# Performance work log

Hardware: AMD Instinct MI355X
Metric: run time of the kernel (lower is better)

Reference implementation:

```python
import jax, jax.numpy as jnp
import numpy as np

B, TE, T = 128, 256, 200
H, PRE, MEL, R = 256, 128, 80, 5
OUT = MEL * R  # 400


def _gru(x, h, wih, whh, bih, bhh):
    # PyTorch GRUCell math. wih: [3H, in], whh: [3H, H]
    gi = x @ wih.T + bih
    gh = h @ whh.T + bhh
    ir, iz, inn = jnp.split(gi, 3, axis=-1)
    hr, hz, hn = jnp.split(gh, 3, axis=-1)
    r = jax.nn.sigmoid(ir + hr)
    z = jax.nn.sigmoid(iz + hz)
    n = jnp.tanh(inn + r * hn)
    return (1.0 - z) * n + z * h


def setup_inputs() -> dict:
    key = jax.random.key(0)
    ks = jax.random.split(key, 32)
    s = 0.05
    d = {
        "encoder_outputs": jax.random.normal(ks[0], (B, TE, H), jnp.float32),
        "targets": jax.random.normal(ks[1], (B, T, OUT), jnp.float32),
        # prenet (note: prenet input is mel_dim*r = 400 frames fed through Linear(400->256)
        # is not in the original; original hardcodes Linear(256,256) on a 400-dim frame --
        # a bug. We size the first prenet layer to the actual frame dim 400.)
        "prenet_w1": jax.random.normal(ks[2], (H, OUT), jnp.float32) * s,
        "prenet_b1": jnp.zeros((H,), jnp.float32),
        "prenet_w2": jax.random.normal(ks[3], (PRE, H), jnp.float32) * s,
        "prenet_b2": jnp.zeros((PRE,), jnp.float32),
        # attention RNN: GRUCell(256+128, 256)
        "attn_wih": jax.random.normal(ks[4], (3 * H, H + PRE), jnp.float32) * s,
        "attn_whh": jax.random.normal(ks[5], (3 * H, H), jnp.float32) * s,
        "attn_bih": jnp.zeros((3 * H,), jnp.float32),
        "attn_bhh": jnp.zeros((3 * H,), jnp.float32),
        # Bahdanau attention: query layer, memory layer (bias-free), score vector v
        "wq": jax.random.normal(ks[6], (H, H), jnp.float32) * s,
        "wm": jax.random.normal(ks[7], (H, H), jnp.float32) * s,
        "v_attn": jax.random.normal(ks[8], (H,), jnp.float32) * s,
        # proj_to_decoder: Linear(512, 256)
        "wp": jax.random.normal(ks[9], (H, 2 * H), jnp.float32) * s,
        "bp": jnp.zeros((H,), jnp.float32),
        # decoder GRUCell x2 (256,256)
        "g1_wih": jax.random.normal(ks[10], (3 * H, H), jnp.float32) * s,
        "g1_whh": jax.random.normal(ks[11], (3 * H, H), jnp.float32) * s,
        "g1_bih": jnp.zeros((3 * H,), jnp.float32),
        "g1_bhh": jnp.zeros((3 * H,), jnp.float32),
        "g2_wih": jax.random.normal(ks[12], (3 * H, H), jnp.float32) * s,
        "g2_whh": jax.random.normal(ks[13], (3 * H, H), jnp.float32) * s,
        "g2_bih": jnp.zeros((3 * H,), jnp.float32),
        "g2_bhh": jnp.zeros((3 * H,), jnp.float32),
        # proj_to_mel: Linear(256, mel_dim*r)
        "wo": jax.random.normal(ks[14], (OUT, H), jnp.float32) * s,
        "bo": jnp.zeros((OUT,), jnp.float32),
    }
    return d


def reference(encoder_outputs, targets, prenet_w1, prenet_b1, prenet_w2, prenet_b2,
              attn_wih, attn_whh, attn_bih, attn_bhh, wq, wm, v_attn, wp, bp,
              g1_wih, g1_whh, g1_bih, g1_bhh, g2_wih, g2_whh, g2_bih, g2_bhh,
              wo, bo):
    b = encoder_outputs.shape[0]
    # precompute processed memory once (original memory_layer)
    pm = encoder_outputs @ wm.T  # [B, Te, H]

    # teacher-forced previous frames: go-frame (zeros) then targets[:, :-1]
    prev = jnp.concatenate([jnp.zeros((b, 1, OUT), encoder_outputs.dtype),
                            targets[:, :-1]], axis=1)  # [B, T, OUT]
    prev = jnp.swapaxes(prev, 0, 1)  # [T, B, OUT]

    def step(carry, frame):
        attn_h, h1, h2, attn_val = carry
        # prenet (dropout in eval mode -> identity)
        p = jax.nn.relu(frame @ prenet_w1.T + prenet_b1)
        p = jax.nn.relu(p @ prenet_w2.T + prenet_b2)  # [B, 128]
        # attention RNN
        x = jnp.concatenate([p, attn_val], axis=-1)  # [B, 384]
        attn_h = _gru(x, attn_h, attn_wih, attn_whh, attn_bih, attn_bhh)
        # Bahdanau additive attention
        q = attn_h @ wq.T  # [B, H]
        e = jnp.einsum('bth,h->bt', jnp.tanh(pm + q[:, None, :]), v_attn)  # [B, Te]
        align = jax.nn.softmax(e, axis=-1)
        attn_val = jnp.einsum('bt,bth->bh', align, encoder_outputs)
        # decoder RNNs with residual connections
        dec_in = jnp.concatenate([attn_h, attn_val], axis=-1) @ wp.T + bp
        h1 = _gru(dec_in, h1, g1_wih, g1_whh, g1_bih, g1_bhh)
        dec_in = h1 + dec_in
        h2 = _gru(dec_in, h2, g2_wih, g2_whh, g2_bih, g2_bhh)
        dec_in = h2 + dec_in
        out = dec_in @ wo.T + bo  # [B, OUT]
        return (attn_h, h1, h2, attn_val), (out, align)

    z = jnp.zeros((b, H), encoder_outputs.dtype)
    init = (z, z, z, z)
    _, (outs, aligns) = jax.lax.scan(step, init, prev)
    outputs = jnp.swapaxes(outs, 0, 1)      # [B, T, mel_dim*r]
    alignments = jnp.swapaxes(aligns, 0, 1)  # [B, T, Te]
    return outputs, alignments
```

## Files before the change

kernel.cpp:

```cpp
#include <hip/hip_runtime.h>

#define B_    128
#define T_    200
#define TE_   256
#define H_    256
#define PRE_  128
#define OUT_  400
#define BT_   (B_*T_)

__device__ __forceinline__ float sigm_(float x){ return 1.f/(1.f+__expf(-x)); }
__device__ __forceinline__ float tanh_(float x){
  x = fminf(15.f, fmaxf(-15.f, x));
  float e = __expf(2.f*x);
  return 1.f - 2.f/(e+1.f);
}
__device__ __forceinline__ float b2f_lo(unsigned u){ return __uint_as_float(u << 16); }
__device__ __forceinline__ float b2f_hi(unsigned u){ return __uint_as_float(u & 0xffff0000u); }
__device__ __forceinline__ unsigned short f2b(float f){
  unsigned u = __float_as_uint(f);
  unsigned r = (u + 0x7fff + ((u >> 16) & 1)) >> 16;
  return (unsigned short)r;
}

#define Q4(xv, wv, A0,A1,A2,A3) \
  A0=fmaf(xv,b2f_lo(wv.x),A0); A1=fmaf(xv,b2f_hi(wv.x),A1); \
  A2=fmaf(xv,b2f_lo(wv.y),A2); A3=fmaf(xv,b2f_hi(wv.y),A3);

struct TD { const float* src; void* dst; int N; int Ksrc; int col0; int Keff; int bf16; int blk0; };
struct TDs { TD d[14]; };

__global__ __launch_bounds__(256) void transpose_cast(TDs P)
{
  int bid = blockIdx.x, m = 0;
#pragma unroll
  for (int i = 1; i < 14; ++i) if (bid >= P.d[i].blk0) m = i;
  TD t = P.d[m];
  long gid = (long)(bid - t.blk0)*256 + threadIdx.x;
  long nk = (long)t.N * t.Keff;
  if (gid >= nk) return;
  int k = (int)(gid / t.N);
  int j = (int)(gid % t.N);
  float v = t.src[(size_t)j*t.Ksrc + t.col0 + k];
  if (t.bf16) ((unsigned short*)t.dst)[(size_t)k*t.N + j] = f2b(v);
  else        ((float*)t.dst)[(size_t)k*t.N + j] = v;
}

template<int AMODE, bool RELU, int OUTMODE>
__global__ __launch_bounds__(256) void gemm_k(const float* __restrict__ A, int lda,
                                              const float* __restrict__ WT, int N, int K,
                                              const float* __restrict__ bias,
                                              float* __restrict__ C)
{
  const int tid  = threadIdx.x;
  const int row0 = blockIdx.x * 64;
  const int n0   = blockIdx.y * 64;
  __shared__ float As[16][68];
  __shared__ float Bs[16][64];
  const int tx = tid & 15, ty = tid >> 4;
  float acc[4][4];
#pragma unroll
  for (int i = 0; i < 4; ++i)
#pragma unroll
    for (int j = 0; j < 4; ++j) acc[i][j] = 0.f;

  for (int k0 = 0; k0 < K; k0 += 16){
#pragma unroll
    for (int l = 0; l < 4; ++l){
      int idx = tid + l*256;
      int m2 = idx >> 4, kk = idx & 15;
      float v;
      if (AMODE == 1){
        int r = row0 + m2;
        int t = r % T_;
        v = (t == 0) ? 0.f : A[(size_t)(r-1)*OUT_ + k0 + kk];
      } else {
        v = A[(size_t)(row0+m2)*lda + k0 + kk];
      }
      As[kk][m2] = v;
    }
#pragma unroll
    for (int l = 0; l < 4; ++l){
      int idx = tid + l*256;
      int kk = idx >> 6, j = idx & 63;
      int jg = n0 + j;
      Bs[kk][j] = (jg < N) ? WT[(size_t)(k0+kk)*N + jg] : 0.f;
    }
    __syncthreads();
#pragma unroll
    for (int kk = 0; kk < 16; ++kk){
      float4 a4 = *(const float4*)&As[kk][ty*4];
      float4 b4 = *(const float4*)&Bs[kk][tx*4];
      acc[0][0] = fmaf(a4.x, b4.x, acc[0][0]); acc[0][1] = fmaf(a4.x, b4.y, acc[0][1]);
      acc[0][2] = fmaf(a4.x, b4.z, acc[0][2]); acc[0][3] = fmaf(a4.x, b4.w, acc[0][3]);
      acc[1][0] = fmaf(a4.y, b4.x, acc[1][0]); acc[1][1] = fmaf(a4.y, b4.y, acc[1][1]);
      acc[1][2] = fmaf(a4.y, b4.z, acc[1][2]); acc[1][3] = fmaf(a4.y, b4.w, acc[1][3]);
      acc[2][0] = fmaf(a4.z, b4.x, acc[2][0]); acc[2][1] = fmaf(a4.z, b4.y, acc[2][1]);
      acc[2][2] = fmaf(a4.z, b4.z, acc[2][2]); acc[2][3] = fmaf(a4.z, b4.w, acc[2][3]);
      acc[3][0] = fmaf(a4.w, b4.x, acc[3][0]); acc[3][1] = fmaf(a4.w, b4.y, acc[3][1]);
      acc[3][2] = fmaf(a4.w, b4.z, acc[3][2]); acc[3][3] = fmaf(a4.w, b4.w, acc[3][3]);
    }
    __syncthreads();
  }
#pragma unroll
  for (int i = 0; i < 4; ++i){
    int r = row0 + ty*4 + i;
#pragma unroll
    for (int jj = 0; jj < 4; ++jj){
      int c = n0 + tx*4 + jj;
      if (c < N){
        float v = acc[i][jj] + (bias ? bias[c] : 0.f);
        if (RELU) v = fmaxf(v, 0.f);
        if (OUTMODE == 0){
          C[(size_t)r*N + c] = v;
        } else if (OUTMODE == 1){
          int b = r / TE_, te = r % TE_;
          C[((size_t)b*H_ + c)*TE_ + te] = v;
        } else {
          int b = r / TE_, te = r % TE_;
          ((unsigned short*)C)[((size_t)b*H_ + c)*TE_ + te] = f2b(v);
        }
      }
    }
  }
}

__device__ __forceinline__ void mv768_pair(const uint2* __restrict__ wA, const uint2* __restrict__ wB,
                                           const float* __restrict__ xA, const float* __restrict__ xB,
                                           float* __restrict__ outA, float* __restrict__ outB,
                                           int kg, int jt)
{
  const float4* xa4 = (const float4*)xA;
  const float4* xb4 = (const float4*)xB;
  const uint2* pA = wA + (size_t)(kg*64)*192 + jt;
  const uint2* pB = wB + (size_t)(kg*64)*192 + jt;
  float a0=0,a1=0,a2=0,a3=0, c0=0,c1=0,c2=0,c3=0;
#pragma unroll 4
  for (int k4 = 0; k4 < 16; ++k4){
    float4 x1 = xa4[kg*16+k4];
    float4 x2 = xb4[kg*16+k4];
    uint2 wa0=pA[0],wa1=pA[192],wa2=pA[384],wa3=pA[576]; pA += 768;
    uint2 wb0=pB[0],wb1=pB[192],wb2=pB[384],wb3=pB[576]; pB += 768;
    Q4(x1.x, wa0, a0,a1,a2,a3) Q4(x1.y, wa1, a0,a1,a2,a3)
    Q4(x1.z, wa2, a0,a1,a2,a3) Q4(x1.w, wa3, a0,a1,a2,a3)
    Q4(x2.x, wb0, c0,c1,c2,c3) Q4(x2.y, wb1, c0,c1,c2,c3)
    Q4(x2.z, wb2, c0,c1,c2,c3) Q4(x2.w, wb3, c0,c1,c2,c3)
  }
  *(float4*)(outA + jt*4) = make_float4(a0,a1,a2,a3);
  *(float4*)(outB + jt*4) = make_float4(c0,c1,c2,c3);
}

__device__ __forceinline__ void mv768_single(const uint2* __restrict__ w,
                                             const float* __restrict__ x,
                                             float* __restrict__ out, int kg, int jt)
{
  const float4* x4 = (const float4*)x;
  const uint2* p = w + (size_t)(kg*64)*192 + jt;
  float a0=0,a1=0,a2=0,a3=0;
#pragma unroll 4
  for (int k4 = 0; k4 < 16; ++k4){
    float4 x1 = x4[kg*16+k4];
    uint2 w0=p[0],w1=p[192],w2=p[384],w3=p[576]; p += 768;
    Q4(x1.x, w0, a0,a1,a2,a3) Q4(x1.y, w1, a0,a1,a2,a3)
    Q4(x1.z, w2, a0,a1,a2,a3) Q4(x1.w, w3, a0,a1,a2,a3)
  }
  *(float4*)(out + jt*4) = make_float4(a0,a1,a2,a3);
}

__device__ __forceinline__ void mv256_pair(const uint2* __restrict__ wA, const uint2* __restrict__ wB,
                                           const float* __restrict__ x,
                                           float* __restrict__ outA, float* __restrict__ outB,
                                           int kg, int jt)
{
  const float4* x4 = (const float4*)x;
  const uint2* pA = wA + (size_t)(kg*16)*64 + jt;
  const uint2* pB = wB + (size_t)(kg*16)*64 + jt;
  float a0=0,a1=0,a2=0,a3=0, c0=0,c1=0,c2=0,c3=0;
#pragma unroll
  for (int k4 = 0; k4 < 4; ++k4){
    float4 x1 = x4[kg*4+k4];
    uint2 wa0=pA[0],wa1=pA[64],wa2=pA[128],wa3=pA[192]; pA += 256;
    uint2 wb0=pB[0],wb1=pB[64],wb2=pB[128],wb3=pB[192]; pB += 256;
    Q4(x1.x, wa0, a0,a1,a2,a3) Q4(x1.y, wa1, a0,a1,a2,a3)
    Q4(x1.z, wa2, a0,a1,a2,a3) Q4(x1.w, wa3, a0,a1,a2,a3)
    Q4(x1.x, wb0, c0,c1,c2,c3) Q4(x1.y, wb1, c0,c1,c2,c3)
    Q4(x1.z, wb2, c0,c1,c2,c3) Q4(x1.w, wb3, c0,c1,c2,c3)
  }
  *(float4*)(outA + jt*4) = make_float4(a0,a1,a2,a3);
  *(float4*)(outB + jt*4) = make_float4(c0,c1,c2,c3);
}

__device__ __forceinline__ void mv256_single(const uint2* __restrict__ w,
                                             const float* __restrict__ x,
                                             float* __restrict__ out, int kg, int jt)
{
  const float4* x4 = (const float4*)x;
  const uint2* p = w + (size_t)(kg*16)*64 + jt;
  float a0=0,a1=0,a2=0,a3=0;
#pragma unroll
  for (int k4 = 0; k4 < 4; ++k4){
    float4 x1 = x4[kg*4+k4];
    uint2 w0=p[0],w1=p[64],w2=p[128],w3=p[192]; p += 256;
    Q4(x1.x, w0, a0,a1,a2,a3) Q4(x1.y, w1, a0,a1,a2,a3)
    Q4(x1.z, w2, a0,a1,a2,a3) Q4(x1.w, w3, a0,a1,a2,a3)
  }
  *(float4*)(out + jt*4) = make_float4(a0,a1,a2,a3);
}

__device__ __forceinline__ float gru_gate(float gi0,float gi1,float gi2,
                                          float gh0,float gh1,float gh2, float hprev){
  float r = sigm_(gi0+gh0);
  float z = sigm_(gi1+gh1);
  float n = tanh_(gi2 + r*gh2);
  return (1.f-z)*n + z*hprev;
}

struct DP {
  const float *preGI;
  const unsigned short *pm16, *enc16;
  const unsigned short *awihA, *awhh, *wq, *wp, *g1wih, *g1whh, *g2wih, *g2whh;
  const float *abhh, *g1bih, *g1bhh, *g2bih, *g2bhh, *bp, *v_attn;
  float *decbuf, *aln;
};

__global__ __launch_bounds__(1024) void decoder_kernel(DP P)
{
  const int tid = threadIdx.x;
  const int b = blockIdx.x;

  __shared__ __align__(16) float s_part[12288];
  __shared__ __align__(16) float s_g1h[768], s_g2h[768];
  __shared__ __align__(16) float s_ah[H_], s_h1[H_], s_h2[H_], s_av[H_], s_dec[H_];
  __shared__ __align__(16) float s_q[H_], s_dq[H_], s_al[TE_], s_v[H_];
  __shared__ __align__(16) float s_preg[768];
  __shared__ float s_red[4];

  float r_bh0=0,r_bh1=0,r_bh2=0, r_1bi0=0,r_1bi1=0,r_1bi2=0;
  float r_2bi0=0,r_2bi1=0,r_2bi2=0, r_bp=0, r_g1bh=0, r_g2bh=0;
  if (tid < H_){
    r_bh0=P.abhh[tid];  r_bh1=P.abhh[H_+tid];  r_bh2=P.abhh[2*H_+tid];
    r_1bi0=P.g1bih[tid]; r_1bi1=P.g1bih[H_+tid]; r_1bi2=P.g1bih[2*H_+tid];
    r_2bi0=P.g2bih[tid]; r_2bi1=P.g2bih[H_+tid]; r_2bi2=P.g2bih[2*H_+tid];
    r_bp=P.bp[tid];
    s_v[tid]=P.v_attn[tid];
    s_ah[tid]=0.f; s_h1[tid]=0.f; s_h2[tid]=0.f; s_av[tid]=0.f;
  } else {
    int j = tid - 256;
    r_g1bh = P.g1bhh[j];
    r_g2bh = P.g2bhh[j];
  }
  __syncthreads();

  const float* preg = P.preGI + (size_t)b*T_*768;
  const uint2* pm2  = (const uint2*)(P.pm16  + (size_t)b*H_*TE_);
  const uint2* en2  = (const uint2*)(P.enc16 + (size_t)b*TE_*H_);
  float* aln_b = P.aln + (size_t)b*T_*TE_;
  float* dec_b = P.decbuf + (size_t)b*T_*H_;

  const uint2* awihA2 = (const uint2*)P.awihA;
  const uint2* awhh2  = (const uint2*)P.awhh;
  const uint2* wq2    = (const uint2*)P.wq;
  const uint2* wpA2   = (const uint2*)P.wp;
  const uint2* wpB2   = ((const uint2*)P.wp) + 16384;
  const uint2* g1wih2 = (const uint2*)P.g1wih;
  const uint2* g1whh2 = (const uint2*)P.g1whh;
  const uint2* g2wih2 = (const uint2*)P.g2wih;
  const uint2* g2whh2 = (const uint2*)P.g2whh;

  const int kg8 = tid >> 6, jt8 = tid & 63;

  for (int t = 0; t < T_; ++t){
    if (tid < 768){
      const int kg = tid / 192, jt = tid - (tid/192)*192;
      mv768_pair(awihA2, awhh2, s_av, s_ah,
                 s_part + (0*4+kg)*768, s_part + (1*4+kg)*768, kg, jt);
      mv768_pair(g1whh2, g2whh2, s_h1, s_h2,
                 s_part + (2*4+kg)*768, s_part + (3*4+kg)*768, kg, jt);
    } else {
      int i = tid - 768;
      s_preg[i]       = preg[(size_t)t*768 + i];
      s_preg[i + 256] = preg[(size_t)t*768 + i + 256];
      s_preg[i + 512] = preg[(size_t)t*768 + i + 512];
    }
    __syncthreads();
    if (tid < H_){
      float gi0 = s_part[tid]     + s_part[768+tid]     + s_part[1536+tid]     + s_part[2304+tid]     + s_preg[tid];
      float gi1 = s_part[256+tid] + s_part[1024+tid]    + s_part[1792+tid]     + s_part[2560+tid]     + s_preg[256+tid];
      float gi2 = s_part[512+tid] + s_part[1280+tid]    + s_part[2048+tid]     + s_part[2816+tid]     + s_preg[512+tid];
      float gh0 = s_part[3072+tid]     + s_part[3840+tid]     + s_part[4608+tid]     + s_part[5376+tid]     + r_bh0;
      float gh1 = s_part[3072+256+tid] + s_part[3840+256+tid] + s_part[4608+256+tid] + s_part[5376+256+tid] + r_bh1;
      float gh2 = s_part[3072+512+tid] + s_part[3840+512+tid] + s_part[4608+512+tid] + s_part[5376+512+tid] + r_bh2;
      s_ah[tid] = gru_gate(gi0,gi1,gi2, gh0,gh1,gh2, s_ah[tid]);
    } else {
      int j = tid - 256;
      s_g1h[j] = s_part[6144+j] + s_part[6912+j] + s_part[7680+j] + s_part[8448+j] + r_g1bh;
      s_g2h[j] = s_part[9216+j] + s_part[9984+j] + s_part[10752+j] + s_part[11520+j] + r_g2bh;
    }
    __syncthreads();

    mv256_pair(wq2, wpA2, s_ah, s_part + kg8*256, s_part + 4096 + kg8*256, kg8, jt8);
    __syncthreads();
    if (tid < 256){
      float q = 0.f;
#pragma unroll
      for (int g = 0; g < 16; ++g) q += s_part[g*256 + tid];
      s_q[tid] = q;
    } else if (tid < 512){
      int j = tid - 256;
      float d = 0.f;
#pragma unroll
      for (int g = 0; g < 16; ++g) d += s_part[4096 + g*256 + j];
      s_dq[j] = d;
    }
    __syncthreads();

    {
      float a0=0,a1=0,a2=0,a3=0;
#pragma unroll 4
      for (int hh = 0; hh < 16; ++hh){
        int h = kg8*16 + hh;
        uint2 pv = pm2[(size_t)h*64 + jt8];
        float qh = s_q[h], vh = s_v[h];
        a0 = fmaf(vh, tanh_(b2f_lo(pv.x)+qh), a0);
        a1 = fmaf(vh, tanh_(b2f_hi(pv.x)+qh), a1);
        a2 = fmaf(vh, tanh_(b2f_lo(pv.y)+qh), a2);
        a3 = fmaf(vh, tanh_(b2f_hi(pv.y)+qh), a3);
      }
      *(float4*)(s_part + kg8*256 + jt8*4) = make_float4(a0,a1,a2,a3);
    }
    __syncthreads();
    float ex = 0.f;
    if (tid < TE_){
      float e = 0.f;
#pragma unroll
      for (int g = 0; g < 16; ++g) e += s_part[g*256 + tid];
      ex = __expf(e);
      float s = ex;
      for (int o = 32; o; o >>= 1) s += __shfl_down(s, o, 64);
      if ((tid & 63) == 0) s_red[tid >> 6] = s;
    }
    __syncthreads();
    if (tid < TE_){
      float s = (s_red[0]+s_red[1])+(s_red[2]+s_red[3]);
      float al = ex / s;
      s_al[tid] = al;
      aln_b[(size_t)t*TE_ + tid] = al;
    }
    __syncthreads();

    {
      float a0=0,a1=0,a2=0,a3=0;
#pragma unroll 4
      for (int tt = 0; tt < 16; ++tt){
        int te = kg8*16 + tt;
        float alv = s_al[te];
        uint2 ev = en2[(size_t)te*64 + jt8];
        a0 = fmaf(alv, b2f_lo(ev.x), a0);
        a1 = fmaf(alv, b2f_hi(ev.x), a1);
        a2 = fmaf(alv, b2f_lo(ev.y), a2);
        a3 = fmaf(alv, b2f_hi(ev.y), a3);
      }
      *(float4*)(s_part + kg8*256 + jt8*4) = make_float4(a0,a1,a2,a3);
    }
    __syncthreads();
    if (tid < H_){
      float av = 0.f;
#pragma unroll
      for (int g = 0; g < 16; ++g) av += s_part[g*256 + tid];
      s_av[tid] = av;
    }
    __syncthreads();

    mv256_single(wpB2, s_av, s_part + kg8*256, kg8, jt8);
    __syncthreads();
    if (tid < H_){
      float d = s_dq[tid] + r_bp;
#pragma unroll
      for (int g = 0; g < 16; ++g) d += s_part[g*256 + tid];
      s_dec[tid] = d;
    }
    __syncthreads();

    if (tid < 768){
      const int kg = tid / 192, jt = tid - (tid/192)*192;
      mv768_single(g1wih2, s_dec, s_part + kg*768, kg, jt);
    }
    __syncthreads();
    if (tid < H_){
      float gi0 = s_part[tid]     + s_part[768+tid]  + s_part[1536+tid] + s_part[2304+tid] + r_1bi0;
      float gi1 = s_part[256+tid] + s_part[1024+tid] + s_part[1792+tid] + s_part[2560+tid] + r_1bi1;
      float gi2 = s_part[512+tid] + s_part[1280+tid] + s_part[2048+tid] + s_part[2816+tid] + r_1bi2;
      float h1n = gru_gate(gi0,gi1,gi2, s_g1h[tid], s_g1h[256+tid], s_g1h[512+tid], s_h1[tid]);
      s_h1[tid] = h1n;
      s_dec[tid] += h1n;
    }
    __syncthreads();

    if (tid < 768){
      const int kg = tid / 192, jt = tid - (tid/192)*192;
      mv768_single(g2wih2, s_dec, s_part + kg*768, kg, jt);
    }
    __syncthreads();
    if (tid < H_){
      float gi0 = s_part[tid]     + s_part[768+tid]  + s_part[1536+tid] + s_part[2304+tid] + r_2bi0;
      float gi1 = s_part[256+tid] + s_part[1024+tid] + s_part[1792+tid] + s_part[2560+tid] + r_2bi1;
      float gi2 = s_part[512+tid] + s_part[1280+tid] + s_part[2048+tid] + s_part[2816+tid] + r_2bi2;
      float h2n = gru_gate(gi0,gi1,gi2, s_g2h[tid], s_g2h[256+tid], s_g2h[512+tid], s_h2[tid]);
      s_h2[tid] = h2n;
      float d = s_dec[tid] + h2n;
      s_dec[tid] = d;
      dec_b[(size_t)t*H_ + tid] = d;
    }
    __syncthreads();
  }
}

extern "C" void kernel_launch(void* const* d_in, const int* in_sizes, int n_in,
                              void* d_out, int out_size, void* d_ws, size_t ws_size,
                              hipStream_t stream)
{
  const float* enc   = (const float*)d_in[0];
  const float* tgt   = (const float*)d_in[1];
  const float* pw1   = (const float*)d_in[2];
  const float* pb1   = (const float*)d_in[3];
  const float* pw2   = (const float*)d_in[4];
  const float* pb2   = (const float*)d_in[5];
  const float* awih  = (const float*)d_in[6];
  const float* awhh  = (const float*)d_in[7];
  const float* abih  = (const float*)d_in[8];
  const float* abhh  = (const float*)d_in[9];
  const float* wq    = (const float*)d_in[10];
  const float* wm    = (const float*)d_in[11];
  const float* vat   = (const float*)d_in[12];
  const float* wp    = (const float*)d_in[13];
  const float* bp    = (const float*)d_in[14];
  const float* g1wih = (const float*)d_in[15];
  const float* g1whh = (const float*)d_in[16];
  const float* g1bih = (const float*)d_in[17];
  const float* g1bhh = (const float*)d_in[18];
  const float* g2wih = (const float*)d_in[19];
  const float* g2whh = (const float*)d_in[20];
  const float* g2bih = (const float*)d_in[21];
  const float* g2bhh = (const float*)d_in[22];
  const float* wo    = (const float*)d_in[23];
  const float* bo    = (const float*)d_in[24];

  float* ws = (float*)d_ws;
  size_t off = 0;
  auto alloc = [&](size_t n){ float* p = ws + off; off += (n + 3) & ~(size_t)3; return p; };

  float* wmT    = alloc(65536);
  float* w1T    = alloc(102400);
  float* w2T    = alloc(32768);
  float* awihPT = alloc(98304);
  float* woT    = alloc(102400);
  unsigned short* awihA16 = (unsigned short*)alloc(98304);
  unsigned short* awhh16  = (unsigned short*)alloc(98304);
  unsigned short* wq16    = (unsigned short*)alloc(32768);
  unsigned short* wp16    = (unsigned short*)alloc(65536);
  unsigned short* g1wih16 = (unsigned short*)alloc(98304);
  unsigned short* g1whh16 = (unsigned short*)alloc(98304);
  unsigned short* g2wih16 = (unsigned short*)alloc(98304);
  unsigned short* g2whh16 = (unsigned short*)alloc(98304);
  unsigned short* pm16  = (unsigned short*)alloc(4194304);
  unsigned short* enc16 = (unsigned short*)alloc(4194304);
  float* decb   = alloc((size_t)BT_*H_);
  float* p2f    = alloc((size_t)BT_*PRE_);
  float* preGIf = alloc((size_t)BT_*3*H_);
  float* p1f = decb;

  TDs td;
  const float* srcs[14] = { wm,  pw1, pw2, awih, wo,  awih, awhh, wq,  wp,  g1wih, g1whh, g2wih, g2whh, enc };
  void* dsts[14] = { wmT, w1T, w2T, awihPT, woT, awihA16, awhh16, wq16, wp16, g1wih16, g1whh16, g2wih16, g2whh16, enc16 };
  int   Ns[14]   = { 256, 256, 128, 768,  400, 768, 768, 256, 256, 768, 768, 768, 768, B_*TE_*H_ };
  int   Kss[14]  = { 256, 400, 256, 384,  256, 384, 256, 256, 512, 256, 256, 256, 256, 1 };
  int   c0s[14]  = { 0,   0,   0,   0,    0,   128, 0,   0,   0,   0,   0,   0,   0,   0 };
  int   Kes[14]  = { 256, 400, 256, 128,  256, 256, 256, 256, 512, 256, 256, 256, 256, 1 };
  int   bfs[14]  = { 0,   0,   0,   0,    0,   1,   1,   1,   1,   1,   1,   1,   1,   1 };
  int blk = 0;
  for (int i = 0; i < 14; ++i){
    td.d[i] = { srcs[i], dsts[i], Ns[i], Kss[i], c0s[i], Kes[i], bfs[i], blk };
    long nk = (long)Ns[i]*Kes[i];
    blk += (int)((nk + 255) / 256);
  }
  transpose_cast<<<blk, 256, 0, stream>>>(td);

  gemm_k<1, true, 0><<<dim3(BT_/64, 4), 256, 0, stream>>>(tgt, 0,   w1T,    256, 400, pb1,  p1f);
  gemm_k<0, true, 0><<<dim3(BT_/64, 2), 256, 0, stream>>>(p1f, 256, w2T,    128, 256, pb2,  p2f);
  gemm_k<0, false,0><<<dim3(BT_/64,12), 256, 0, stream>>>(p2f, 128, awihPT, 768, 128, abih, preGIf);
  gemm_k<0, false,2><<<dim3((B_*TE_)/64, 4), 256, 0, stream>>>(enc, 256, wmT, 256, 256, nullptr, (float*)pm16);

  DP P;
  P.preGI = preGIf; P.pm16 = pm16; P.enc16 = enc16;
  P.awihA = awihA16; P.awhh = awhh16; P.wq = wq16; P.wp = wp16;
  P.g1wih = g1wih16; P.g1whh = g1whh16; P.g2wih = g2wih16; P.g2whh = g2whh16;
  P.abhh = abhh; P.g1bih = g1bih; P.g1bhh = g1bhh; P.g2bih = g2bih; P.g2bhh = g2bhh;
  P.bp = bp; P.v_attn = vat;
  P.decbuf = decb;
  P.aln = (float*)d_out + (size_t)BT_*OUT_;
  decoder_kernel<<<B_, 1024, 0, stream>>>(P);

  gemm_k<0, false,0><<<dim3(BT_/64, 7), 256, 0, stream>>>(decb, 256, woT, 400, 256, bo, (float*)d_out);
}
```

Before: 14.44 ms.

## Repack bf16 weights, memory and encoder into k-pair interleaved uint4 tiles

Replaces the per-matrix bf16 transposes with new pack kernels. These interleave two k-rows per 16-byte word, so the decoder's matvecs, attention score and context loops issue full uint4 loads with all loads hoisted ahead of the FMAs. Pointer offsets are precomputed outside the time loop, and the decoder gets a launch_bounds occupancy hint. The aim is to cut load instruction count and latency stalls in the latency-bound recurrent kernel, at the cost of more live registers and more complex packing indices.

```diff
diff --git a/kernel.cpp b/kernel.cpp
--- a/kernel.cpp
+++ b/kernel.cpp
@@ -22,27 +22,143 @@
   return (unsigned short)r;
 }
 
-#define Q4(xv, wv, A0,A1,A2,A3) \
-  A0=fmaf(xv,b2f_lo(wv.x),A0); A1=fmaf(xv,b2f_hi(wv.x),A1); \
-  A2=fmaf(xv,b2f_lo(wv.y),A2); A3=fmaf(xv,b2f_hi(wv.y),A3);
-
-struct TD { const float* src; void* dst; int N; int Ksrc; int col0; int Keff; int bf16; int blk0; };
-struct TDs { TD d[14]; };
+
+__device__ __forceinline__ void pk8(float&a0,float&a1,float&a2,float&a3,
+                                    const uint4 w, const float x0, const float x1){
+  a0=fmaf(x0,b2f_lo(w.x),a0); a1=fmaf(x0,b2f_hi(w.x),a1);
+  a2=fmaf(x0,b2f_lo(w.y),a2); a3=fmaf(x0,b2f_hi(w.y),a3);
+  a0=fmaf(x1,b2f_lo(w.z),a0); a1=fmaf(x1,b2f_hi(w.z),a1);
+  a2=fmaf(x1,b2f_lo(w.w),a2); a3=fmaf(x1,b2f_hi(w.w),a3);
+}
+
+__device__ __forceinline__ void mv768_pair(const uint4* __restrict__ pA, const uint4* __restrict__ pB,
+                                           const float* __restrict__ xA, const float* __restrict__ xB,
+                                           float* __restrict__ outA, float* __restrict__ outB, int jt)
+{
+  float A0=0,A1=0,A2=0,A3=0, B0=0,B1=0,B2=0,B3=0;
+#pragma unroll
+  for (int blk = 0; blk < 4; ++blk){
+    const uint4* qA = pA + blk*1536;
+    const uint4* qB = pB + blk*1536;
+    uint4 a0=qA[0],a1=qA[192],a2=qA[384],a3=qA[576],a4=qA[768],a5=qA[960],a6=qA[1152],a7=qA[1344];
+    uint4 b0=qB[0],b1=qB[192],b2=qB[384],b3=qB[576],b4=qB[768],b5=qB[960],b6=qB[1152],b7=qB[1344];
+    float4 xa0=*(const float4*)(xA+blk*16),   xa1=*(const float4*)(xA+blk*16+4);
+    float4 xa2=*(const float4*)(xA+blk*16+8), xa3=*(const float4*)(xA+blk*16+12);
+    float4 xb0=*(const float4*)(xB+blk*16),   xb1=*(const float4*)(xB+blk*16+4);
+    float4 xb2=*(const float4*)(xB+blk*16+8), xb3=*(const float4*)(xB+blk*16+12);
+    pk8(A0,A1,A2,A3, a0, xa0.x,xa0.y); pk8(A0,A1,A2,A3, a1, xa0.z,xa0.w);
+    pk8(A0,A1,A2,A3, a2, xa1.x,xa1.y); pk8(A0,A1,A2,A3, a3, xa1.z,xa1.w);
+    pk8(A0,A1,A2,A3, a4, xa2.x,xa2.y); pk8(A0,A1,A2,A3, a5, xa2.z,xa2.w);
+    pk8(A0,A1,A2,A3, a6, xa3.x,xa3.y); pk8(A0,A1,A2,A3, a7, xa3.z,xa3.w);
+    pk8(B0,B1,B2,B3, b0, xb0.x,xb0.y); pk8(B0,B1,B2,B3, b1, xb0.z,xb0.w);
+    pk8(B0,B1,B2,B3, b2, xb1.x,xb1.y); pk8(B0,B1,B2,B3, b3, xb1.z,xb1.w);
+    pk8(B0,B1,B2,B3, b4, xb2.x,xb2.y); pk8(B0,B1,B2,B3, b5, xb2.z,xb2.w);
+    pk8(B0,B1,B2,B3, b6, xb3.x,xb3.y); pk8(B0,B1,B2,B3, b7, xb3.z,xb3.w);
+  }
+  *(float4*)(outA + jt*4) = make_float4(A0,A1,A2,A3);
+  *(float4*)(outB + jt*4) = make_float4(B0,B1,B2,B3);
+}
+
+__device__ __forceinline__ void mv768_single(const uint4* __restrict__ pA,
+                                             const float* __restrict__ xA,
+                                             float* __restrict__ outA, int jt)
+{
+  float A0=0,A1=0,A2=0,A3=0;
+#pragma unroll
+  for (int blk = 0; blk < 4; ++blk){
+    const uint4* qA = pA + blk*1536;
+    uint4 a0=qA[0],a1=qA[192],a2=qA[384],a3=qA[576],a4=qA[768],a5=qA[960],a6=qA[1152],a7=qA[1344];
+    float4 xa0=*(const float4*)(xA+blk*16),   xa1=*(const float4*)(xA+blk*16+4);
+    float4 xa2=*(const float4*)(xA+blk*16+8), xa3=*(const float4*)(xA+blk*16+12);
+    pk8(A0,A1,A2,A3, a0, xa0.x,xa0.y); pk8(A0,A1,A2,A3, a1, xa0.z,xa0.w);
+    pk8(A0,A1,A2,A3, a2, xa1.x,xa1.y); pk8(A0,A1,A2,A3, a3, xa1.z,xa1.w);
+    pk8(A0,A1,A2,A3, a4, xa2.x,xa2.y); pk8(A0,A1,A2,A3, a5, xa2.z,xa2.w);
+    pk8(A0,A1,A2,A3, a6, xa3.x,xa3.y); pk8(A0,A1,A2,A3, a7, xa3.z,xa3.w);
+  }
+  *(float4*)(outA + jt*4) = make_float4(A0,A1,A2,A3);
+}
+
+__device__ __forceinline__ void mv256_pair(const uint4* __restrict__ pA, const uint4* __restrict__ pB,
+                                           const float* __restrict__ x,
+                                           float* __restrict__ outA, float* __restrict__ outB, int jt)
+{
+  uint4 a0=pA[0],a1=pA[64],a2=pA[128],a3=pA[192],a4=pA[256],a5=pA[320],a6=pA[384],a7=pA[448];
+  uint4 b0=pB[0],b1=pB[64],b2=pB[128],b3=pB[192],b4=pB[256],b5=pB[320],b6=pB[384],b7=pB[448];
+  float4 x0=*(const float4*)(x), x1=*(const float4*)(x+4);
+  float4 x2=*(const float4*)(x+8), x3=*(const float4*)(x+12);
+  float A0=0,A1=0,A2=0,A3=0, B0=0,B1=0,B2=0,B3=0;
+  pk8(A0,A1,A2,A3, a0, x0.x,x0.y); pk8(A0,A1,A2,A3, a1, x0.z,x0.w);
+  pk8(A0,A1,A2,A3, a2, x1.x,x1.y); pk8(A0,A1,A2,A3, a3, x1.z,x1.w);
+  pk8(A0,A1,A2,A3, a4, x2.x,x2.y); pk8(A0,A1,A2,A3, a5, x2.z,x2.w);
+  pk8(A0,A1,A2,A3, a6, x3.x,x3.y); pk8(A0,A1,A2,A3, a7, x3.z,x3.w);
+  pk8(B0,B1,B2,B3, b0, x0.x,x0.y); pk8(B0,B1,B2,B3, b1, x0.z,x0.w);
+  pk8(B0,B1,B2,B3, b2, x1.x,x1.y); pk8(B0,B1,B2,B3, b3, x1.z,x1.w);
+  pk8(B0,B1,B2,B3, b4, x2.x,x2.y); pk8(B0,B1,B2,B3, b5, x2.z,x2.w);
+  pk8(B0,B1,B2,B3, b6, x3.x,x3.y); pk8(B0,B1,B2,B3, b7, x3.z,x3.w);
+  *(float4*)(outA + jt*4) = make_float4(A0,A1,A2,A3);
+  *(float4*)(outB + jt*4) = make_float4(B0,B1,B2,B3);
+}
+
+__device__ __forceinline__ void mv256_single(const uint4* __restrict__ pA,
+                                             const float* __restrict__ x,
+                                             float* __restrict__ outA, int jt)
+{
+  uint4 a0=pA[0],a1=pA[64],a2=pA[128],a3=pA[192],a4=pA[256],a5=pA[320],a6=pA[384],a7=pA[448];
+  float4 x0=*(const float4*)(x), x1=*(const float4*)(x+4);
+  float4 x2=*(const float4*)(x+8), x3=*(const float4*)(x+12);
+  float A0=0,A1=0,A2=0,A3=0;
+  pk8(A0,A1,A2,A3, a0, x0.x,x0.y); pk8(A0,A1,A2,A3, a1, x0.z,x0.w);
+  pk8(A0,A1,A2,A3, a2, x1.x,x1.y); pk8(A0,A1,A2,A3, a3, x1.z,x1.w);
+  pk8(A0,A1,A2,A3, a4, x2.x,x2.y); pk8(A0,A1,A2,A3, a5, x2.z,x2.w);
+  pk8(A0,A1,A2,A3, a6, x3.x,x3.y); pk8(A0,A1,A2,A3, a7, x3.z,x3.w);
+  *(float4*)(outA + jt*4) = make_float4(A0,A1,A2,A3);
+}
+
+struct TD { const float* src; float* dst; int N; int Ksrc; int col0; int Keff; int blk0; };
+struct TDs { TD d[5]; };
 
 __global__ __launch_bounds__(256) void transpose_cast(TDs P)
 {
   int bid = blockIdx.x, m = 0;
 #pragma unroll
-  for (int i = 1; i < 14; ++i) if (bid >= P.d[i].blk0) m = i;
+  for (int i = 1; i < 5; ++i) if (bid >= P.d[i].blk0) m = i;
   TD t = P.d[m];
   long gid = (long)(bid - t.blk0)*256 + threadIdx.x;
   long nk = (long)t.N * t.Keff;
   if (gid >= nk) return;
   int k = (int)(gid / t.N);
   int j = (int)(gid % t.N);
-  float v = t.src[(size_t)j*t.Ksrc + t.col0 + k];
-  if (t.bf16) ((unsigned short*)t.dst)[(size_t)k*t.N + j] = f2b(v);
-  else        ((float*)t.dst)[(size_t)k*t.N + j] = v;
+  t.dst[(size_t)k*t.N + j] = t.src[(size_t)j*t.Ksrc + t.col0 + k];
+}
+
+struct WP { const float* src; int dstoff_u4; int fmt3; int col0; int srcK; int blk0; };
+struct WPs { WP d[9]; };
+
+__global__ __launch_bounds__(256) void wpack(WPs P, unsigned short* __restrict__ dst)
+{
+  int bid = blockIdx.x, m = 0;
+#pragma unroll
+  for (int i = 1; i < 9; ++i) if (bid >= P.d[i].blk0) m = i;
+  WP t = P.d[m];
+  int idx = (bid - t.blk0)*256 + threadIdx.x;
+  int total = t.fmt3 ? 196608 : 65536;
+  if (idx >= total) return;
+  int kp, jq, w8;
+  if (t.fmt3){ kp = idx/1536; int rem = idx - kp*1536; jq = rem>>3; w8 = rem&7; }
+  else       { kp = idx>>9;   int rem = idx&511;       jq = rem>>3; w8 = rem&7; }
+  int k = kp*2 + (w8>>2);
+  int j = jq*4 + (w8&3);
+  dst[(size_t)t.dstoff_u4*8 + idx] = f2b(t.src[(size_t)j*t.srcK + t.col0 + k]);
+}
+
+__global__ __launch_bounds__(256) void encpack(const float* __restrict__ enc, unsigned short* __restrict__ dst)
+{
+  size_t gid = (size_t)blockIdx.x*256 + threadIdx.x;
+  int b  = (int)(gid >> 16);
+  int te = (int)(gid >> 8) & 255;
+  int h  = (int)gid & 255;
+  float v = enc[gid];
+  dst[(size_t)b*65536 + (size_t)(te>>1)*512 + (h>>2)*8 + (te&1)*4 + (h&3)] = f2b(v);
 }
 
 template<int AMODE, bool RELU, int OUTMODE>
@@ -65,8 +181,8 @@
 
   for (int k0 = 0; k0 < K; k0 += 16){
 #pragma unroll
-    for (int l = 0; l < 4; ++l){
-      int idx = tid + l*256;
+    for (int ll = 0; ll < 4; ++ll){
+      int idx = tid + ll*256;
       int m2 = idx >> 4, kk = idx & 15;
       float v;
       if (AMODE == 1){
@@ -79,8 +195,8 @@
       As[kk][m2] = v;
     }
 #pragma unroll
-    for (int l = 0; l < 4; ++l){
-      int idx = tid + l*256;
+    for (int ll = 0; ll < 4; ++ll){
+      int idx = tid + ll*256;
       int kk = idx >> 6, j = idx & 63;
       int jg = n0 + j;
       Bs[kk][j] = (jg < N) ? WT[(size_t)(k0+kk)*N + jg] : 0.f;
@@ -112,117 +228,24 @@
         if (RELU) v = fmaxf(v, 0.f);
         if (OUTMODE == 0){
           C[(size_t)r*N + c] = v;
-        } else if (OUTMODE == 1){
-          int b = r / TE_, te = r % TE_;
-          C[((size_t)b*H_ + c)*TE_ + te] = v;
         } else {
-          int b = r / TE_, te = r % TE_;
-          ((unsigned short*)C)[((size_t)b*H_ + c)*TE_ + te] = f2b(v);
+          int bb = r >> 8, te = r & 255, h = c;
+          ((unsigned short*)C)[(size_t)bb*65536 + (size_t)(h>>1)*512 + (te>>2)*8
+                               + (h&1)*4 + (te&3)] = f2b(v);
         }
       }
     }
   }
 }
 
-__device__ __forceinline__ void mv768_pair(const uint2* __restrict__ wA, const uint2* __restrict__ wB,
-                                           const float* __restrict__ xA, const float* __restrict__ xB,
-                                           float* __restrict__ outA, float* __restrict__ outB,
-                                           int kg, int jt)
-{
-  const float4* xa4 = (const float4*)xA;
-  const float4* xb4 = (const float4*)xB;
-  const uint2* pA = wA + (size_t)(kg*64)*192 + jt;
-  const uint2* pB = wB + (size_t)(kg*64)*192 + jt;
-  float a0=0,a1=0,a2=0,a3=0, c0=0,c1=0,c2=0,c3=0;
-#pragma unroll 4
-  for (int k4 = 0; k4 < 16; ++k4){
-    float4 x1 = xa4[kg*16+k4];
-    float4 x2 = xb4[kg*16+k4];
-    uint2 wa0=pA[0],wa1=pA[192],wa2=pA[384],wa3=pA[576]; pA += 768;
-    uint2 wb0=pB[0],wb1=pB[192],wb2=pB[384],wb3=pB[576]; pB += 768;
-    Q4(x1.x, wa0, a0,a1,a2,a3) Q4(x1.y, wa1, a0,a1,a2,a3)
-    Q4(x1.z, wa2, a0,a1,a2,a3) Q4(x1.w, wa3, a0,a1,a2,a3)
-    Q4(x2.x, wb0, c0,c1,c2,c3) Q4(x2.y, wb1, c0,c1,c2,c3)
-    Q4(x2.z, wb2, c0,c1,c2,c3) Q4(x2.w, wb3, c0,c1,c2,c3)
-  }
-  *(float4*)(outA + jt*4) = make_float4(a0,a1,a2,a3);
-  *(float4*)(outB + jt*4) = make_float4(c0,c1,c2,c3);
-}
-
-__device__ __forceinline__ void mv768_single(const uint2* __restrict__ w,
-                                             const float* __restrict__ x,
-                                             float* __restrict__ out, int kg, int jt)
-{
-  const float4* x4 = (const float4*)x;
-  const uint2* p = w + (size_t)(kg*64)*192 + jt;
-  float a0=0,a1=0,a2=0,a3=0;
-#pragma unroll 4
-  for (int k4 = 0; k4 < 16; ++k4){
-    float4 x1 = x4[kg*16+k4];
-    uint2 w0=p[0],w1=p[192],w2=p[384],w3=p[576]; p += 768;
-    Q4(x1.x, w0, a0,a1,a2,a3) Q4(x1.y, w1, a0,a1,a2,a3)
-    Q4(x1.z, w2, a0,a1,a2,a3) Q4(x1.w, w3, a0,a1,a2,a3)
-  }
-  *(float4*)(out + jt*4) = make_float4(a0,a1,a2,a3);
-}
-
-__device__ __forceinline__ void mv256_pair(const uint2* __restrict__ wA, const uint2* __restrict__ wB,
-                                           const float* __restrict__ x,
-                                           float* __restrict__ outA, float* __restrict__ outB,
-                                           int kg, int jt)
-{
-  const float4* x4 = (const float4*)x;
-  const uint2* pA = wA + (size_t)(kg*16)*64 + jt;
-  const uint2* pB = wB + (size_t)(kg*16)*64 + jt;
-  float a0=0,a1=0,a2=0,a3=0, c0=0,c1=0,c2=0,c3=0;
-#pragma unroll
-  for (int k4 = 0; k4 < 4; ++k4){
-    float4 x1 = x4[kg*4+k4];
-    uint2 wa0=pA[0],wa1=pA[64],wa2=pA[128],wa3=pA[192]; pA += 256;
-    uint2 wb0=pB[0],wb1=pB[64],wb2=pB[128],wb3=pB[192]; pB += 256;
-    Q4(x1.x, wa0, a0,a1,a2,a3) Q4(x1.y, wa1, a0,a1,a2,a3)
-    Q4(x1.z, wa2, a0,a1,a2,a3) Q4(x1.w, wa3, a0,a1,a2,a3)
-    Q4(x1.x, wb0, c0,c1,c2,c3) Q4(x1.y, wb1, c0,c1,c2,c3)
-    Q4(x1.z, wb2, c0,c1,c2,c3) Q4(x1.w, wb3, c0,c1,c2,c3)
-  }
-  *(float4*)(outA + jt*4) = make_float4(a0,a1,a2,a3);
-  *(float4*)(outB + jt*4) = make_float4(c0,c1,c2,c3);
-}
-
-__device__ __forceinline__ void mv256_single(const uint2* __restrict__ w,
-                                             const float* __restrict__ x,
-                                             float* __restrict__ out, int kg, int jt)
-{
-  const float4* x4 = (const float4*)x;
-  const uint2* p = w + (size_t)(kg*16)*64 + jt;
-  float a0=0,a1=0,a2=0,a3=0;
-#pragma unroll
-  for (int k4 = 0; k4 < 4; ++k4){
-    float4 x1 = x4[kg*4+k4];
-    uint2 w0=p[0],w1=p[64],w2=p[128],w3=p[192]; p += 256;
-    Q4(x1.x, w0, a0,a1,a2,a3) Q4(x1.y, w1, a0,a1,a2,a3)
-    Q4(x1.z, w2, a0,a1,a2,a3) Q4(x1.w, w3, a0,a1,a2,a3)
-  }
-  *(float4*)(out + jt*4) = make_float4(a0,a1,a2,a3);
-}
-
-__device__ __forceinline__ float gru_gate(float gi0,float gi1,float gi2,
-                                          float gh0,float gh1,float gh2, float hprev){
-  float r = sigm_(gi0+gh0);
-  float z = sigm_(gi1+gh1);
-  float n = tanh_(gi2 + r*gh2);
-  return (1.f-z)*n + z*hprev;
-}
-
 struct DP {
   const float *preGI;
-  const unsigned short *pm16, *enc16;
-  const unsigned short *awihA, *awhh, *wq, *wp, *g1wih, *g1whh, *g2wih, *g2whh;
+  const uint4 *wpk, *pmpk, *encpk;
   const float *abhh, *g1bih, *g1bhh, *g2bih, *g2bhh, *bp, *v_attn;
   float *decbuf, *aln;
 };
 
-__global__ __launch_bounds__(1024) void decoder_kernel(DP P)
+__global__ __launch_bounds__(1024, 4) void decoder_kernel(DP P)
 {
   const int tid = threadIdx.x;
   const int b = blockIdx.x;
@@ -251,30 +274,31 @@
   __syncthreads();
 
   const float* preg = P.preGI + (size_t)b*T_*768;
-  const uint2* pm2  = (const uint2*)(P.pm16  + (size_t)b*H_*TE_);
-  const uint2* en2  = (const uint2*)(P.enc16 + (size_t)b*TE_*H_);
-  float* aln_b = P.aln + (size_t)b*T_*TE_;
+  float* aln_b = P.aln    + (size_t)b*T_*TE_;
   float* dec_b = P.decbuf + (size_t)b*T_*H_;
 
-  const uint2* awihA2 = (const uint2*)P.awihA;
-  const uint2* awhh2  = (const uint2*)P.awhh;
-  const uint2* wq2    = (const uint2*)P.wq;
-  const uint2* wpA2   = (const uint2*)P.wp;
-  const uint2* wpB2   = ((const uint2*)P.wp) + 16384;
-  const uint2* g1wih2 = (const uint2*)P.g1wih;
-  const uint2* g1whh2 = (const uint2*)P.g1whh;
-  const uint2* g2wih2 = (const uint2*)P.g2wih;
-  const uint2* g2whh2 = (const uint2*)P.g2whh;
-
+  const int kg7 = (tid < 768) ? tid/192 : 3;
+  const int jt7 = (tid < 768) ? (tid - (tid/192)*192) : 0;
   const int kg8 = tid >> 6, jt8 = tid & 63;
+
+  const uint4* pAW = P.wpk +      0 + kg7*6144 + jt7;
+  const uint4* pAH = P.wpk +  24576 + kg7*6144 + jt7;
+  const uint4* pG1 = P.wpk +  49152 + kg7*6144 + jt7;
+  const uint4* pG2 = P.wpk +  73728 + kg7*6144 + jt7;
+  const uint4* pI1 = P.wpk +  98304 + kg7*6144 + jt7;
+  const uint4* pI2 = P.wpk + 122880 + kg7*6144 + jt7;
+  const uint4* pQ  = P.wpk + 147456 + kg8*512 + jt8;
+  const uint4* pPA = P.wpk + 155648 + kg8*512 + jt8;
+  const uint4* pPB = P.wpk + 163840 + kg8*512 + jt8;
+  const uint4* pPM = P.pmpk  + (size_t)b*8192 + kg8*512 + jt8;
+  const uint4* pEN = P.encpk + (size_t)b*8192 + kg8*512 + jt8;
 
   for (int t = 0; t < T_; ++t){
     if (tid < 768){
-      const int kg = tid / 192, jt = tid - (tid/192)*192;
-      mv768_pair(awihA2, awhh2, s_av, s_ah,
-                 s_part + (0*4+kg)*768, s_part + (1*4+kg)*768, kg, jt);
-      mv768_pair(g1whh2, g2whh2, s_h1, s_h2,
-                 s_part + (2*4+kg)*768, s_part + (3*4+kg)*768, kg, jt);
+      mv768_pair(pAW, pAH, s_av + kg7*64, s_ah + kg7*64,
+                 s_part + (0*4+kg7)*768, s_part + (1*4+kg7)*768, jt7);
+      mv768_pair(pG1, pG2, s_h1 + kg7*64, s_h2 + kg7*64,
+                 s_part + (2*4+kg7)*768, s_part + (3*4+kg7)*768, jt7);
     } else {
       int i = tid - 768;
       s_preg[i]       = preg[(size_t)t*768 + i];
@@ -289,7 +313,8 @@
       float gh0 = s_part[3072+tid]     + s_part[3840+tid]     + s_part[4608+tid]     + s_part[5376+tid]     + r_bh0;
       float gh1 = s_part[3072+256+tid] + s_part[3840+256+tid] + s_part[4608+256+tid] + s_part[5376+256+tid] + r_bh1;
       float gh2 = s_part[3072+512+tid] + s_part[3840+512+tid] + s_part[4608+512+tid] + s_part[5376+512+tid] + r_bh2;
-      s_ah[tid] = gru_gate(gi0,gi1,gi2, gh0,gh1,gh2, s_ah[tid]);
+      float r = sigm_(gi0+gh0), z = sigm_(gi1+gh1), n = tanh_(gi2 + r*gh2);
+      s_ah[tid] = (1.f-z)*n + z*s_ah[tid];
     } else {
       int j = tid - 256;
       s_g1h[j] = s_part[6144+j] + s_part[6912+j] + s_part[7680+j] + s_part[8448+j] + r_g1bh;
@@ -297,7 +322,7 @@
     }
     __syncthreads();
 
-    mv256_pair(wq2, wpA2, s_ah, s_part + kg8*256, s_part + 4096 + kg8*256, kg8, jt8);
+    mv256_pair(pQ, pPA, s_ah + kg8*16, s_part + kg8*256, s_part + 4096 + kg8*256, jt8);
     __syncthreads();
     if (tid < 256){
       float q = 0.f;
@@ -314,17 +339,17 @@
     __syncthreads();
 
     {
+      uint4 w0=pPM[0],w1=pPM[64],w2=pPM[128],w3=pPM[192],w4=pPM[256],w5=pPM[320],w6=pPM[384],w7=pPM[448];
       float a0=0,a1=0,a2=0,a3=0;
-#pragma unroll 4
-      for (int hh = 0; hh < 16; ++hh){
-        int h = kg8*16 + hh;
-        uint2 pv = pm2[(size_t)h*64 + jt8];
-        float qh = s_q[h], vh = s_v[h];
-        a0 = fmaf(vh, tanh_(b2f_lo(pv.x)+qh), a0);
-        a1 = fmaf(vh, tanh_(b2f_hi(pv.x)+qh), a1);
-        a2 = fmaf(vh, tanh_(b2f_lo(pv.y)+qh), a2);
-        a3 = fmaf(vh, tanh_(b2f_hi(pv.y)+qh), a3);
-      }
+      int h0 = kg8*16;
+#define SC(wv, hh) { float q0=s_q[hh], v0=s_v[hh], q1=s_q[(hh)+1], v1=s_v[(hh)+1]; \
+      a0 = fmaf(v0, tanh_(b2f_lo(wv.x)+q0), a0); a1 = fmaf(v0, tanh_(b2f_hi(wv.x)+q0), a1); \
+      a2 = fmaf(v0, tanh_(b2f_lo(wv.y)+q0), a2); a3 = fmaf(v0, tanh_(b2f_hi(wv.y)+q0), a3); \
+      a0 = fmaf(v1, tanh_(b2f_lo(wv.z)+q1), a0); a1 = fmaf(v1, tanh_(b2f_hi(wv.z)+q1), a1); \
+      a2 = fmaf(v1, tanh_(b2f_lo(wv.w)+q1), a2); a3 = fmaf(v1, tanh_(b2f_hi(wv.w)+q1), a3); }
+      SC(w0,h0) SC(w1,h0+2) SC(w2,h0+4) SC(w3,h0+6)
+      SC(w4,h0+8) SC(w5,h0+10) SC(w6,h0+12) SC(w7,h0+14)
+#undef SC
       *(float4*)(s_part + kg8*256 + jt8*4) = make_float4(a0,a1,a2,a3);
     }
     __syncthreads();
@@ -348,17 +373,17 @@
     __syncthreads();
 
     {
+      uint4 w0=pEN[0],w1=pEN[64],w2=pEN[128],w3=pEN[192],w4=pEN[256],w5=pEN[320],w6=pEN[384],w7=pEN[448];
       float a0=0,a1=0,a2=0,a3=0;
-#pragma unroll 4
-      for (int tt = 0; tt < 16; ++tt){
-        int te = kg8*16 + tt;
-        float alv = s_al[te];
-        uint2 ev = en2[(size_t)te*64 + jt8];
-        a0 = fmaf(alv, b2f_lo(ev.x), a0);
-        a1 = fmaf(alv, b2f_hi(ev.x), a1);
-        a2 = fmaf(alv, b2f_lo(ev.y), a2);
-        a3 = fmaf(alv, b2f_hi(ev.y), a3);
-      }
+      int t0 = kg8*16;
+#define CT(wv, tt) { float l0=s_al[tt], l1=s_al[(tt)+1]; \
+      a0 = fmaf(l0, b2f_lo(wv.x), a0); a1 = fmaf(l0, b2f_hi(wv.x), a1); \
+      a2 = fmaf(l0, b2f_lo(wv.y), a2); a3 = fmaf(l0, b2f_hi(wv.y), a3); \
+      a0 = fmaf(l1, b2f_lo(wv.z), a0); a1 = fmaf(l1, b2f_hi(wv.z), a1); \
+      a2 = fmaf(l1, b2f_lo(wv.w), a2); a3 = fmaf(l1, b2f_hi(wv.w), a3); }
+      CT(w0,t0) CT(w1,t0+2) CT(w2,t0+4) CT(w3,t0+6)
+      CT(w4,t0+8) CT(w5,t0+10) CT(w6,t0+12) CT(w7,t0+14)
+#undef CT
       *(float4*)(s_part + kg8*256 + jt8*4) = make_float4(a0,a1,a2,a3);
     }
     __syncthreads();
@@ -370,7 +395,7 @@
     }
     __syncthreads();
 
-    mv256_single(wpB2, s_av, s_part + kg8*256, kg8, jt8);
+    mv256_single(pPB, s_av + kg8*16, s_part + kg8*256, jt8);
     __syncthreads();
     if (tid < H_){
       float d = s_dq[tid] + r_bp;
@@ -381,30 +406,32 @@
     __syncthreads();
 
     if (tid < 768){
-      const int kg = tid / 192, jt = tid - (tid/192)*192;
-      mv768_single(g1wih2, s_dec, s_part + kg*768, kg, jt);
+      mv768_single(pI1, s_dec + kg7*64, s_part + kg7*768, jt7);
     }
     __syncthreads();
     if (tid < H_){
       float gi0 = s_part[tid]     + s_part[768+tid]  + s_part[1536+tid] + s_part[2304+tid] + r_1bi0;
       float gi1 = s_part[256+tid] + s_part[1024+tid] + s_part[1792+tid] + s_part[2560+tid] + r_1bi1;
       float gi2 = s_part[512+tid] + s_part[1280+tid] + s_part[2048+tid] + s_part[2816+tid] + r_1bi2;
-      float h1n = gru_gate(gi0,gi1,gi2, s_g1h[tid], s_g1h[256+tid], s_g1h[512+tid], s_h1[tid]);
+      float r = sigm_(gi0 + s_g1h[tid]), z = sigm_(gi1 + s_g1h[256+tid]);
+      float n = tanh_(gi2 + r*s_g1h[512+tid]);
+      float h1n = (1.f-z)*n + z*s_h1[tid];
       s_h1[tid] = h1n;
       s_dec[tid] += h1n;
     }
     __syncthreads();
 
     if (tid < 768){
-      const int kg = tid / 192, jt = tid - (tid/192)*192;
-      mv768_single(g2wih2, s_dec, s_part + kg*768, kg, jt);
+      mv768_single(pI2, s_dec + kg7*64, s_part + kg7*768, jt7);
     }
     __syncthreads();
     if (tid < H_){
       float gi0 = s_part[tid]     + s_part[768+tid]  + s_part[1536+tid] + s_part[2304+tid] + r_2bi0;
       float gi1 = s_part[256+tid] + s_part[1024+tid] + s_part[1792+tid] + s_part[2560+tid] + r_2bi1;
       float gi2 = s_part[512+tid] + s_part[1280+tid] + s_part[2048+tid] + s_part[2816+tid] + r_2bi2;
-      float h2n = gru_gate(gi0,gi1,gi2, s_g2h[tid], s_g2h[256+tid], s_g2h[512+tid], s_h2[tid]);
+      float r = sigm_(gi0 + s_g2h[tid]), z = sigm_(gi1 + s_g2h[256+tid]);
+      float n = tanh_(gi2 + r*s_g2h[512+tid]);
+      float h2n = (1.f-z)*n + z*s_h2[tid];
       s_h2[tid] = h2n;
       float d = s_dec[tid] + h2n;
       s_dec[tid] = d;
@@ -453,51 +480,56 @@
   float* w2T    = alloc(32768);
   float* awihPT = alloc(98304);
   float* woT    = alloc(102400);
-  unsigned short* awihA16 = (unsigned short*)alloc(98304);
-  unsigned short* awhh16  = (unsigned short*)alloc(98304);
-  unsigned short* wq16    = (unsigned short*)alloc(32768);
-  unsigned short* wp16    = (unsigned short*)alloc(65536);
-  unsigned short* g1wih16 = (unsigned short*)alloc(98304);
-  unsigned short* g1whh16 = (unsigned short*)alloc(98304);
-  unsigned short* g2wih16 = (unsigned short*)alloc(98304);
-  unsigned short* g2whh16 = (unsigned short*)alloc(98304);
-  unsigned short* pm16  = (unsigned short*)alloc(4194304);
-  unsigned short* enc16 = (unsigned short*)alloc(4194304);
+  float* wpkf   = alloc(688128);
+  float* pmpkf  = alloc(4194304);
+  float* encpkf = alloc(4194304);
   float* decb   = alloc((size_t)BT_*H_);
   float* p2f    = alloc((size_t)BT_*PRE_);
   float* preGIf = alloc((size_t)BT_*3*H_);
   float* p1f = decb;
 
   TDs td;
-  const float* srcs[14] = { wm,  pw1, pw2, awih, wo,  awih, awhh, wq,  wp,  g1wih, g1whh, g2wih, g2whh, enc };
-  void* dsts[14] = { wmT, w1T, w2T, awihPT, woT, awihA16, awhh16, wq16, wp16, g1wih16, g1whh16, g2wih16, g2whh16, enc16 };
-  int   Ns[14]   = { 256, 256, 128, 768,  400, 768, 768, 256, 256, 768, 768, 768, 768, B_*TE_*H_ };
-  int   Kss[14]  = { 256, 400, 256, 384,  256, 384, 256, 256, 512, 256, 256, 256, 256, 1 };
-  int   c0s[14]  = { 0,   0,   0,   0,    0,   128, 0,   0,   0,   0,   0,   0,   0,   0 };
-  int   Kes[14]  = { 256, 400, 256, 128,  256, 256, 256, 256, 512, 256, 256, 256, 256, 1 };
-  int   bfs[14]  = { 0,   0,   0,   0,    0,   1,   1,   1,   1,   1,   1,   1,   1,   1 };
+  const float* tsr[5] = { wm,  pw1, pw2, awih, wo  };
+  float* tds[5]       = { wmT, w1T, w2T, awihPT, woT };
+  int   tN[5]  = { 256, 256, 128, 768, 400 };
+  int   tK[5]  = { 256, 400, 256, 384, 256 };
+  int   tc[5]  = { 0,   0,   0,   0,   0   };
+  int   tE[5]  = { 256, 400, 256, 128, 256 };
   int blk = 0;
-  for (int i = 0; i < 14; ++i){
-    td.d[i] = { srcs[i], dsts[i], Ns[i], Kss[i], c0s[i], Kes[i], bfs[i], blk };
-    long nk = (long)Ns[i]*Kes[i];
-    blk += (int)((nk + 255) / 256);
+  for (int i = 0; i < 5; ++i){
+    td.d[i] = { tsr[i], tds[i], tN[i], tK[i], tc[i], tE[i], blk };
+    blk += (int)(((long)tN[i]*tE[i] + 255) / 256);
   }
   transpose_cast<<<blk, 256, 0, stream>>>(td);
 
-  gemm_k<1, true, 0><<<dim3(BT_/64, 4), 256, 0, stream>>>(tgt, 0,   w1T,    256, 400, pb1,  p1f);
-  gemm_k<0, true, 0><<<dim3(BT_/64, 2), 256, 0, stream>>>(p1f, 256, w2T,    128, 256, pb2,  p2f);
-  gemm_k<0, false,0><<<dim3(BT_/64,12), 256, 0, stream>>>(p2f, 128, awihPT, 768, 128, abih, preGIf);
-  gemm_k<0, false,2><<<dim3((B_*TE_)/64, 4), 256, 0, stream>>>(enc, 256, wmT, 256, 256, nullptr, (float*)pm16);
+  WPs wp_;
+  const float* wsr[9] = { awih,  awhh,  g1whh, g2whh, g1wih, g2wih,  wq,     wp,     wp };
+  int wdo[9] = { 0,     24576, 49152, 73728, 98304, 122880, 147456, 155648, 163840 };
+  int wf3[9] = { 1,     1,     1,     1,     1,     1,      0,      0,      0 };
+  int wc0[9] = { 128,   0,     0,     0,     0,     0,      0,      0,      256 };
+  int wsk[9] = { 384,   256,   256,   256,   256,   256,    256,    512,    512 };
+  int wblk = 0;
+  for (int i = 0; i < 9; ++i){
+    wp_.d[i] = { wsr[i], wdo[i], wf3[i], wc0[i], wsk[i], wblk };
+    wblk += (wf3[i] ? 196608 : 65536) / 256;
+  }
+  wpack<<<wblk, 256, 0, stream>>>(wp_, (unsigned short*)wpkf);
+
+  encpack<<<(B_*TE_*H_)/256, 256, 0, stream>>>(enc, (unsigned short*)encpkf);
+
+  gemm_k<1, true,  0><<<dim3(BT_/64, 4), 256, 0, stream>>>(tgt, 0,   w1T,    256, 400, pb1,  p1f);
+  gemm_k<0, true,  0><<<dim3(BT_/64, 2), 256, 0, stream>>>(p1f, 256, w2T,    128, 256, pb2,  p2f);
+  gemm_k<0, false, 0><<<dim3(BT_/64,12), 256, 0, stream>>>(p2f, 128, awihPT, 768, 128, abih, preGIf);
+  gemm_k<0, false, 3><<<dim3((B_*TE_)/64, 4), 256, 0, stream>>>(enc, 256, wmT, 256, 256, nullptr, pmpkf);
 
   DP P;
-  P.preGI = preGIf; P.pm16 = pm16; P.enc16 = enc16;
-  P.awihA = awihA16; P.awhh = awhh16; P.wq = wq16; P.wp = wp16;
-  P.g1wih = g1wih16; P.g1whh = g1whh16; P.g2wih = g2wih16; P.g2whh = g2whh16;
+  P.preGI = preGIf;
+  P.wpk = (const uint4*)wpkf; P.pmpk = (const uint4*)pmpkf; P.encpk = (const uint4*)encpkf;
   P.abhh = abhh; P.g1bih = g1bih; P.g1bhh = g1bhh; P.g2bih = g2bih; P.g2bhh = g2bhh;
   P.bp = bp; P.v_attn = vat;
   P.decbuf = decb;
   P.aln = (float*)d_out + (size_t)BT_*OUT_;
   decoder_kernel<<<B_, 1024, 0, stream>>>(P);
 
-  gemm_k<0, false,0><<<dim3(BT_/64, 7), 256, 0, stream>>>(decb, 256, woT, 400, 256, bo, (float*)d_out);
-}
+  gemm_k<0, false, 0><<<dim3(BT_/64, 7), 256, 0, stream>>>(decb, 256, woT, 400, 256, bo, (float*)d_out);
+}
```

Result: slower. 26.92 ms (+86.5%).
